# Performance work log

Measured on AMD Instinct MI355X. Metric: run time of the kernel, lower is better.

Reference implementation:

```python
import jax, jax.numpy as jnp
import numpy as np

M, K, N = 4096, 4096, 11008  # tokens, in_features, out_features


def setup_inputs() -> dict:
    key = jax.random.key(0)
    k1, k2, k3, k4 = jax.random.split(key, 4)
    x = jax.random.normal(k1, (M, K), dtype=jnp.float32)
    weight = jax.random.randint(k2, (N, K), -128, 128).astype(jnp.int8)
    # per-output-channel scale, small positive values as from real quantization
    weight_scale = (jax.random.uniform(k3, (N,), dtype=jnp.float32) * 0.01 + 1e-4)
    bias = jax.random.normal(k4, (N,), dtype=jnp.float32)
    return {"x": x, "weight": weight, "weight_scale": weight_scale, "bias": bias}


def reference(x, weight, weight_scale, bias):
    # Dynamic per-token symmetric quantization of activations to int8.
    x_scale = jnp.max(jnp.abs(x), axis=-1, keepdims=True) / 127.0  # [M, 1]
    x_scale = jnp.maximum(x_scale, 1e-8)
    x_q = jnp.clip(jnp.round(x / x_scale), -128, 127).astype(jnp.int8)  # [M, K]
    acc = jax.lax.dot_general(
        x_q, weight,
        dimension_numbers=(((1,), (1,)), ((), ())),
        preferred_element_type=jnp.int32,
    )
    # Dequantize: per-token activation scale * per-channel weight scale, add bias.
    out = acc.astype(jnp.float32) * x_scale * weight_scale[None, :] + bias[None, :]
    return out
```

## Files before the change

### kernel.cpp

```cpp
#include <hip/hip_runtime.h>
#include <stdint.h>

#define M_DIM 4096
#define K_DIM 4096
#define N_DIM 11008

typedef int v4i __attribute__((ext_vector_type(4)));

#define LDSP(p) ((__attribute__((address_space(3))) void*)(uintptr_t)(p))
#define GLBP(p) ((__attribute__((address_space(1))) void*)(uintptr_t)(p))

__global__ __launch_bounds__(256) void quant_rows(const float* __restrict__ x,
                                                  int8_t* __restrict__ xq,
                                                  float* __restrict__ xs_out) {
    const int row = blockIdx.x;
    const int t = threadIdx.x;
    const float4* xr = (const float4*)(x + (size_t)row * K_DIM);

    float4 v[4];
    float amax = 0.0f;
#pragma unroll
    for (int r = 0; r < 4; ++r) {
        v[r] = xr[t + r * 256];
        amax = fmaxf(amax, fmaxf(fmaxf(fabsf(v[r].x), fabsf(v[r].y)),
                                 fmaxf(fabsf(v[r].z), fabsf(v[r].w))));
    }
#pragma unroll
    for (int off = 32; off > 0; off >>= 1)
        amax = fmaxf(amax, __shfl_xor(amax, off));

    __shared__ float smax[4];
    if ((t & 63) == 0) smax[t >> 6] = amax;
    __syncthreads();
    amax = fmaxf(fmaxf(smax[0], smax[1]), fmaxf(smax[2], smax[3]));

    const float xs = fmaxf(amax / 127.0f, 1e-8f);
    if (t == 0) xs_out[row] = xs;

    int* qo = (int*)(xq + (size_t)row * K_DIM);
#pragma unroll
    for (int r = 0; r < 4; ++r) {
        int q0 = (int)rintf(v[r].x / xs);
        int q1 = (int)rintf(v[r].y / xs);
        int q2 = (int)rintf(v[r].z / xs);
        int q3 = (int)rintf(v[r].w / xs);
        q0 = min(127, max(-128, q0));
        q1 = min(127, max(-128, q1));
        q2 = min(127, max(-128, q2));
        q3 = min(127, max(-128, q3));
        int packed = (q0 & 255) | ((q1 & 255) << 8) | ((q2 & 255) << 16) | (q3 << 24);
        qo[t + r * 256] = packed;
    }
}

__global__ __launch_bounds__(256) void prep_weight(const void* __restrict__ wraw,
                                                   int8_t* __restrict__ w8) {
    const int* wi = (const int*)wraw;
    int c = 0;
#pragma unroll
    for (int i = 0; i < 64; ++i) {
        int w = wi[i];
        c += (w >= -128 && w <= 127) ? 1 : 0;
    }
    const size_t tid = (size_t)blockIdx.x * 256 + threadIdx.x;
    if (c >= 32) {
        union { int4 v; char b[16]; } o;
#pragma unroll
        for (int g = 0; g < 4; ++g) {
            int4 w = ((const int4*)wraw)[tid * 4 + g];
            o.b[g * 4 + 0] = (char)w.x;
            o.b[g * 4 + 1] = (char)w.y;
            o.b[g * 4 + 2] = (char)w.z;
            o.b[g * 4 + 3] = (char)w.w;
        }
        ((int4*)w8)[tid] = o.v;
    } else {
        ((int4*)w8)[tid] = ((const int4*)wraw)[tid];
    }
}

__global__ __launch_bounds__(512, 2) void w8a8_gemm(const int8_t* __restrict__ xq,
                                                    const float* __restrict__ xscale,
                                                    const int8_t* __restrict__ wgt,
                                                    const float* __restrict__ wscale,
                                                    const float* __restrict__ bias,
                                                    float* __restrict__ out) {
    __shared__ __align__(16) int8_t lds_a[3][32768];
    __shared__ __align__(16) int8_t lds_b[2][32768];

    const int t = threadIdx.x;
    const int lane = t & 63;
    const int wave = t >> 6;
    const int wm = wave >> 2;
    const int wn = wave & 3;
    const int quad = lane >> 4;
    const int l15 = lane & 15;

    const int wg = blockIdx.x;
    const int xcd = wg & 7;
    const int u = wg >> 3;
    const int bm = 2 * xcd + (u & 1);
    const int bn = u >> 1;

    const int8_t* pa = xq + (size_t)bm * 256 * K_DIM;
    const int8_t* pb = wgt + (size_t)bn * 256 * K_DIM;

    const int srow = t >> 3;
    const size_t soff = (size_t)srow * K_DIM + (size_t)(((t & 7) ^ (srow & 7)) << 4);
    const size_t g64 = (size_t)64 * K_DIM;

#define STAGE_TILE(gb, lb)                                                                   \
    do {                                                                                     \
        __builtin_amdgcn_global_load_lds(GLBP((gb) + soff), LDSP((lb) + t * 16), 16, 0, 0);  \
        __builtin_amdgcn_global_load_lds(GLBP((gb) + soff + g64), LDSP((lb) + 8192 + t * 16), 16, 0, 0); \
        __builtin_amdgcn_global_load_lds(GLBP((gb) + soff + 2 * g64), LDSP((lb) + 16384 + t * 16), 16, 0, 0); \
        __builtin_amdgcn_global_load_lds(GLBP((gb) + soff + 3 * g64), LDSP((lb) + 24576 + t * 16), 16, 0, 0); \
    } while (0)

    int abase[2], bbase[2];
#pragma unroll
    for (int ks = 0; ks < 2; ++ks) {
        const int ar = wm * 128 + l15;
        abase[ks] = ar * 128 + (((ks * 4 + quad) ^ (l15 & 7)) << 4);
        const int br = wn * 64 + l15;
        bbase[ks] = br * 128 + (((ks * 4 + quad) ^ (l15 & 7)) << 4);
    }

    v4i acc[8][4] = {};
    v4i afA[4], afB[4], bf[8];

#define READ_B4(SB, KS, B0)                                           \
    _Pragma("unroll") for (int j = 0; j < 4; ++j)                     \
        bf[(B0) + j] = *(const v4i*)(&lds_b[SB][bbase[KS] + j * 2048]);
#define READ_AQ(DST, SA, KS, I0)                                      \
    _Pragma("unroll") for (int i = 0; i < 4; ++i)                     \
        DST[i] = *(const v4i*)(&lds_a[SA][abase[KS] + ((I0) + i) * 2048]);
#define MFMA4(AF, B0, R0)                                             \
    __builtin_amdgcn_s_setprio(1);                                    \
    _Pragma("unroll") for (int i = 0; i < 4; ++i)                     \
    _Pragma("unroll") for (int j = 0; j < 4; ++j)                     \
        acc[(R0) + i][j] = __builtin_amdgcn_mfma_i32_16x16x64_i8(     \
            AF[i], bf[(B0) + j], acc[(R0) + i][j], 0, 0, 0);          \
    __builtin_amdgcn_s_setprio(0);
#define LGKM0                                                         \
    asm volatile("s_waitcnt lgkmcnt(0)" ::: "memory");                \
    __builtin_amdgcn_sched_barrier(0);

    STAGE_TILE(pa, &lds_a[0][0]);
    STAGE_TILE(pb, &lds_b[0][0]);
    STAGE_TILE(pa + 128, &lds_a[1][0]);
    STAGE_TILE(pb + 128, &lds_b[1][0]);
    asm volatile("s_waitcnt vmcnt(8)" ::: "memory");
    __builtin_amdgcn_s_barrier();
    READ_B4(0, 0, 0);
    READ_B4(0, 1, 4);
    READ_AQ(afA, 0, 0, 0);
    LGKM0;

#define DO_TILE(U)                                                       \
    {                                                                    \
        constexpr int SA = (U) % 3;                                      \
        constexpr int SB = (U) % 2;                                      \
        constexpr int SA1 = ((U) + 1) % 3;                               \
        constexpr int SB1 = ((U) + 1) % 2;                               \
        constexpr int SA2 = ((U) + 2) % 3;                               \
        const size_t k2 = (size_t)(t0 + (U) + 2) * 128;                  \
        STAGE_TILE(pa + k2, &lds_a[SA2][0]);                             \
        READ_AQ(afB, SA, 0, 4);                                          \
        MFMA4(afA, 0, 0);                                                \
        LGKM0;                                                           \
        READ_AQ(afA, SA, 1, 0);                                          \
        MFMA4(afB, 0, 4);                                                \
        LGKM0;                                                           \
        READ_AQ(afB, SA, 1, 4);                                          \
        MFMA4(afA, 4, 0);                                                \
        LGKM0;                                                           \
        asm volatile("s_waitcnt vmcnt(4)" ::: "memory");                 \
        __builtin_amdgcn_s_barrier();                                    \
        STAGE_TILE(pb + k2, &lds_b[SB][0]);                              \
        READ_B4(SB1, 0, 0);                                              \
        READ_AQ(afA, SA1, 0, 0);                                         \
        MFMA4(afB, 4, 4);                                                \
        READ_B4(SB1, 1, 4);                                              \
        LGKM0;                                                           \
    }

#pragma unroll 1
    for (int t0 = 0; t0 < 30; t0 += 6) {
        DO_TILE(0)
        DO_TILE(1)
        DO_TILE(2)
        DO_TILE(3)
        DO_TILE(4)
        DO_TILE(5)
    }
    READ_AQ(afB, 0, 0, 4);
    MFMA4(afA, 0, 0);
    LGKM0;
    READ_AQ(afA, 0, 1, 0);
    MFMA4(afB, 0, 4);
    LGKM0;
    READ_AQ(afB, 0, 1, 4);
    MFMA4(afA, 4, 0);
    LGKM0;
    asm volatile("s_waitcnt vmcnt(0)" ::: "memory");
    __builtin_amdgcn_s_barrier();
    READ_B4(1, 0, 0);
    READ_AQ(afA, 1, 0, 0);
    MFMA4(afB, 4, 4);
    READ_B4(1, 1, 4);
    LGKM0;
    READ_AQ(afB, 1, 0, 4);
    MFMA4(afA, 0, 0);
    LGKM0;
    READ_AQ(afA, 1, 1, 0);
    MFMA4(afB, 0, 4);
    LGKM0;
    READ_AQ(afB, 1, 1, 4);
    MFMA4(afA, 4, 0);
    LGKM0;
    MFMA4(afB, 4, 4);

    float wsc[4], bi[4];
#pragma unroll
    for (int j = 0; j < 4; ++j) {
        const int cc = bn * 256 + wn * 64 + j * 16 + l15;
        wsc[j] = wscale[cc];
        bi[j] = bias[cc];
    }
#pragma unroll
    for (int i = 0; i < 8; ++i) {
        const int m0 = bm * 256 + wm * 128 + i * 16 + quad * 4;
        const float4 xs4 = *(const float4*)(xscale + m0);
        const float xsv[4] = {xs4.x, xs4.y, xs4.z, xs4.w};
#pragma unroll
        for (int r = 0; r < 4; ++r) {
            const size_t off = (size_t)(m0 + r) * N_DIM + (size_t)bn * 256 + wn * 64 + l15;
#pragma unroll
            for (int j = 0; j < 4; ++j) {
                out[off + j * 16] = (float)acc[i][j][r] * xsv[r] * wsc[j] + bi[j];
            }
        }
    }
}

extern "C" void kernel_launch(void* const* d_in, const int* in_sizes, int n_in,
                              void* d_out, int out_size, void* d_ws, size_t ws_size,
                              hipStream_t stream) {
    const float* x = (const float*)d_in[0];
    const void* wraw = (const void*)d_in[1];
    const float* wscale = (const float*)d_in[2];
    const float* bias = (const float*)d_in[3];
    float* out = (float*)d_out;

    int8_t* w8 = (int8_t*)d_ws;
    int8_t* xq = (int8_t*)d_ws + (size_t)N_DIM * K_DIM;
    float* xs = (float*)((char*)d_ws + (size_t)N_DIM * K_DIM + (size_t)M_DIM * K_DIM);

    quant_rows<<<M_DIM, 256, 0, stream>>>(x, xq, xs);
    prep_weight<<<(N_DIM * (K_DIM / 16)) / 256, 256, 0, stream>>>(wraw, w8);
    w8a8_gemm<<<688, 512, 0, stream>>>(xq, xs, w8, wscale, bias, out);
}
```

Before: 490.4 us.

## Use partial lgkmcnt waits and reorder LDS fragment reads in the GEMM loop

```diff
diff --git a/kernel.cpp b/kernel.cpp
--- a/kernel.cpp
+++ b/kernel.cpp
@@ -129,10 +129,10 @@
     v4i acc[8][4] = {};
     v4i afA[4], afB[4], bf[8];
 
-#define READ_B4(SB, KS, B0)                                           \
+#define ISSUE_B4(SB, KS, B0)                                          \
     _Pragma("unroll") for (int j = 0; j < 4; ++j)                     \
         bf[(B0) + j] = *(const v4i*)(&lds_b[SB][bbase[KS] + j * 2048]);
-#define READ_AQ(DST, SA, KS, I0)                                      \
+#define ISSUE_A4(DST, SA, KS, I0)                                     \
     _Pragma("unroll") for (int i = 0; i < 4; ++i)                     \
         DST[i] = *(const v4i*)(&lds_a[SA][abase[KS] + ((I0) + i) * 2048]);
 #define MFMA4(AF, B0, R0)                                             \
@@ -142,8 +142,8 @@
         acc[(R0) + i][j] = __builtin_amdgcn_mfma_i32_16x16x64_i8(     \
             AF[i], bf[(B0) + j], acc[(R0) + i][j], 0, 0, 0);          \
     __builtin_amdgcn_s_setprio(0);
-#define LGKM0                                                         \
-    asm volatile("s_waitcnt lgkmcnt(0)" ::: "memory");                \
+#define LGKM(n)                                                       \
+    asm volatile("s_waitcnt lgkmcnt(" #n ")" ::: "memory");           \
     __builtin_amdgcn_sched_barrier(0);
 
     STAGE_TILE(pa, &lds_a[0][0]);
@@ -152,10 +152,8 @@
     STAGE_TILE(pb + 128, &lds_b[1][0]);
     asm volatile("s_waitcnt vmcnt(8)" ::: "memory");
     __builtin_amdgcn_s_barrier();
-    READ_B4(0, 0, 0);
-    READ_B4(0, 1, 4);
-    READ_AQ(afA, 0, 0, 0);
-    LGKM0;
+    ISSUE_B4(0, 0, 0);
+    ISSUE_A4(afA, 0, 0, 0);
 
 #define DO_TILE(U)                                                       \
     {                                                                    \
@@ -165,24 +163,28 @@
         constexpr int SB1 = ((U) + 1) % 2;                               \
         constexpr int SA2 = ((U) + 2) % 3;                               \
         const size_t k2 = (size_t)(t0 + (U) + 2) * 128;                  \
+                                                        \
         STAGE_TILE(pa + k2, &lds_a[SA2][0]);                             \
-        READ_AQ(afB, SA, 0, 4);                                          \
-        MFMA4(afA, 0, 0);                                                \
-        LGKM0;                                                           \
-        READ_AQ(afA, SA, 1, 0);                                          \
-        MFMA4(afB, 0, 4);                                                \
-        LGKM0;                                                           \
-        READ_AQ(afB, SA, 1, 4);                                          \
-        MFMA4(afA, 4, 0);                                                \
-        LGKM0;                                                           \
-        asm volatile("s_waitcnt vmcnt(4)" ::: "memory");                 \
+        ISSUE_B4(SB, 1, 4);                                  \
+        ISSUE_A4(afB, SA, 0, 4);                                \
+        LGKM(8);                                \
+        MFMA4(afA, 0, 0);                                    \
+        ISSUE_A4(afA, SA, 1, 0);                                \
+        LGKM(4);                                      \
+        MFMA4(afB, 0, 4);                                    \
+                                                        \
         __builtin_amdgcn_s_barrier();                                    \
         STAGE_TILE(pb + k2, &lds_b[SB][0]);                              \
-        READ_B4(SB1, 0, 0);                                              \
-        READ_AQ(afA, SA1, 0, 0);                                         \
-        MFMA4(afB, 4, 4);                                                \
-        READ_B4(SB1, 1, 4);                                              \
-        LGKM0;                                                           \
+        ISSUE_A4(afB, SA, 1, 4);                                \
+        LGKM(4);                                          \
+        MFMA4(afA, 4, 0);                                    \
+                                                        \
+        asm volatile("s_waitcnt vmcnt(8)" ::: "memory");                 \
+        __builtin_amdgcn_s_barrier();                                    \
+        ISSUE_B4(SB1, 0, 0);                               \
+        ISSUE_A4(afA, SA1, 0, 0);                          \
+        LGKM(8);                                          \
+        MFMA4(afB, 4, 4);                                    \
     }
 
 #pragma unroll 1
@@ -194,31 +196,33 @@
         DO_TILE(4)
         DO_TILE(5)
     }
-    READ_AQ(afB, 0, 0, 4);
+    ISSUE_B4(0, 1, 4);
+    ISSUE_A4(afB, 0, 0, 4);
+    LGKM(8);
     MFMA4(afA, 0, 0);
-    LGKM0;
-    READ_AQ(afA, 0, 1, 0);
+    ISSUE_A4(afA, 0, 1, 0);
+    LGKM(4);
     MFMA4(afB, 0, 4);
-    LGKM0;
-    READ_AQ(afB, 0, 1, 4);
+    ISSUE_A4(afB, 0, 1, 4);
+    LGKM(4);
     MFMA4(afA, 4, 0);
-    LGKM0;
     asm volatile("s_waitcnt vmcnt(0)" ::: "memory");
     __builtin_amdgcn_s_barrier();
-    READ_B4(1, 0, 0);
-    READ_AQ(afA, 1, 0, 0);
+    ISSUE_B4(1, 0, 0);
+    ISSUE_A4(afA, 1, 0, 0);
+    LGKM(8);
     MFMA4(afB, 4, 4);
-    READ_B4(1, 1, 4);
-    LGKM0;
-    READ_AQ(afB, 1, 0, 4);
+    ISSUE_B4(1, 1, 4);
+    ISSUE_A4(afB, 1, 0, 4);
+    LGKM(8);
     MFMA4(afA, 0, 0);
-    LGKM0;
-    READ_AQ(afA, 1, 1, 0);
+    ISSUE_A4(afA, 1, 1, 0);
+    LGKM(4);
     MFMA4(afB, 0, 4);
-    LGKM0;
-    READ_AQ(afB, 1, 1, 4);
+    ISSUE_A4(afB, 1, 1, 4);
+    LGKM(4);
     MFMA4(afA, 4, 0);
-    LGKM0;
+    LGKM(0);
     MFMA4(afB, 4, 4);
 
     float wsc[4], bi[4];
```

After: 492.5 us. No clear change (+0.4%).
